# Performance work log

Measured on AMD Instinct MI355X. Metric: run time of the kernel, lower is better.

Reference implementation:

```python
import jax, jax.numpy as jnp
import numpy as np

B, S, H, E, K = 4, 2048, 1024, 8, 2
DFF = H * 8 // 3  # 2730, as in up: Linear(H, H*8//3)


def setup_inputs() -> dict:
    key = jax.random.key(0)
    ks = jax.random.split(key, 6)
    s = lambda fan: 1.0 / np.sqrt(fan)
    return {
        "x": jax.random.normal(ks[0], (B, S, H), jnp.float32),
        "Wr": jax.random.normal(ks[1], (H, E), jnp.float32) * s(H),
        "br": jnp.zeros((E,), jnp.float32),
        "Wg": jax.random.normal(ks[2], (E, H, H), jnp.float32) * s(H),
        "bg": jnp.zeros((E, H), jnp.float32),
        "Wu": jax.random.normal(ks[3], (E, H, DFF), jnp.float32) * s(H),
        "bu": jnp.zeros((E, DFF), jnp.float32),
        "Wd": jax.random.normal(ks[4], (E, DFF, H), jnp.float32) * s(DFF),
        "bd": jnp.zeros((E, H), jnp.float32),
    }


def reference(x, Wr, br, Wg, bg, Wu, bu, Wd, bd):
    b, s_, h = x.shape
    n = b * s_
    # Router: logits -> softmax -> top-k -> renormalize top-k weights
    expert_weight = x @ Wr + br                      # [B,S,E] (returned raw logits)
    logits_flat = expert_weight.reshape(n, -1)       # [N,E]
    probs = jax.nn.softmax(logits_flat, axis=-1)
    w, idx = jax.lax.top_k(probs, K)                 # [N,K]
    w = w / w.sum(axis=-1, keepdims=True)
    # Scatter top-k weights into dense [N,E] combine matrix (zeros elsewhere)
    rw = jnp.zeros_like(logits_flat).at[jnp.arange(n)[:, None], idx].add(w)
    # Expert MLP (BasicExpert): down(silu(up(gate(x)))); dropout is identity at eval
    xf = x.reshape(n, h)                             # [N,H]
    g = jnp.einsum("nh,ehf->enf", xf, Wg) + bg[:, None, :]       # [E,N,H]
    u = jax.nn.silu(jnp.einsum("enf,efd->end", g, Wu) + bu[:, None, :])  # [E,N,DFF]
    d = jnp.einsum("end,edh->enh", u, Wd) + bd[:, None, :]       # [E,N,H]
    # Combine: weighted sum over experts (weight is 0 for non-selected experts)
    y = jnp.einsum("enh,ne->nh", d, rw)
    return y.reshape(b, s_, h), expert_weight
```

## Files before the change

### kernel.cpp

```cpp
#include <hip/hip_runtime.h>
#include <hip/hip_bf16.h>

#define NB 4
#define SS 2048
#define HH 1024
#define EE 8
#define KK 2
#define DFF 2730
#define DFFP 2752
#define NT (NB*SS)
#define NA (NT*KK)
#define YSZ ((size_t)NT*HH)

using bf16x8 = __attribute__((ext_vector_type(8))) short;
using f32x4  = __attribute__((ext_vector_type(4))) float;

__device__ __forceinline__ ushort f2bf(float f) {
  unsigned u = __float_as_uint(f);
  unsigned r = (u + 0x7FFFu + ((u >> 16) & 1u)) >> 16;
  return (ushort)r;
}

__device__ __forceinline__ void gload16(const ushort* g, ushort* s) {
  __builtin_amdgcn_global_load_lds((const __attribute__((address_space(1))) void*)g,
                                   (__attribute__((address_space(3))) void*)s, 16, 0, 0);
}

__global__ __launch_bounds__(256) void cvt_w_kernel(const float4* __restrict__ in4,
                                                    ushort4* __restrict__ o4, int n4) {
  int i = blockIdx.x * 256 + threadIdx.x;
  if (i >= n4) return;
  float4 v = in4[i];
  ushort4 o;
  o.x = f2bf(v.x); o.y = f2bf(v.y); o.z = f2bf(v.z); o.w = f2bf(v.w);
  o4[i] = o;
}

__global__ __launch_bounds__(256) void transpose_cvt_kernel(
    const float* __restrict__ in, ushort* __restrict__ out,
    int K, int Nn, int Kpad, int Nnpad, long in_estride, long out_estride) {
  __shared__ float t[64][65];
  int e = blockIdx.z;
  const float* ine = in + (size_t)e * in_estride;
  ushort* oute = out + (size_t)e * out_estride;
  int nb = blockIdx.x * 64, kb = blockIdx.y * 64;
  int tid = threadIdx.x;
  int rr = tid >> 4, cc = (tid & 15) * 4;
  if (kb + 64 <= K && nb + 64 <= Nn) {
#pragma unroll
    for (int i = 0; i < 4; ++i) {
      int r = rr + i * 16;
      const float* src = ine + (size_t)(kb + r) * Nn + nb + cc;
      float2 a = *(const float2*)src;
      float2 b = *(const float2*)(src + 2);
      t[r][cc] = a.x; t[r][cc + 1] = a.y; t[r][cc + 2] = b.x; t[r][cc + 3] = b.y;
    }
  } else {
#pragma unroll
    for (int i = 0; i < 4; ++i) {
      int r = rr + i * 16;
      int kg = kb + r;
#pragma unroll
      for (int j = 0; j < 4; ++j) {
        int ng = nb + cc + j;
        t[r][cc + j] = (kg < K && ng < Nn) ? ine[(size_t)kg * Nn + ng] : 0.0f;
      }
    }
  }
  __syncthreads();
  int kq = tid & 15;
#pragma unroll
  for (int i = 0; i < 4; ++i) {
    int nl = rr + i * 16, ng = nb + nl;
    ushort4 v;
    v.x = f2bf(t[kq * 4 + 0][nl]);
    v.y = f2bf(t[kq * 4 + 1][nl]);
    v.z = f2bf(t[kq * 4 + 2][nl]);
    v.w = f2bf(t[kq * 4 + 3][nl]);
    *(ushort4*)&oute[(size_t)ng * Kpad + kb + kq * 4] = v;
  }
}

__global__ __launch_bounds__(256) void router_kernel(
    const float* __restrict__ x, const float* __restrict__ Wr, const float* __restrict__ br,
    float* __restrict__ logits_out, int* __restrict__ counts,
    int* __restrict__ tok_e, float* __restrict__ tok_w, ushort* __restrict__ xb) {
  int wv = threadIdx.x >> 6, l = threadIdx.x & 63;
  int n = blockIdx.x * 4 + wv;
  const float* xr = x + (size_t)n * HH;
  ushort* xbr = xb + (size_t)n * HH;
  float acc[8] = {0, 0, 0, 0, 0, 0, 0, 0};
#pragma unroll 4
  for (int i = 0; i < 16; ++i) {
    int k = l + i * 64;
    float xv = xr[k];
    xbr[k] = f2bf(xv);
    const float4* w4 = (const float4*)(Wr + (size_t)k * 8);
    float4 a = w4[0], b = w4[1];
    acc[0] += xv * a.x; acc[1] += xv * a.y; acc[2] += xv * a.z; acc[3] += xv * a.w;
    acc[4] += xv * b.x; acc[5] += xv * b.y; acc[6] += xv * b.z; acc[7] += xv * b.w;
  }
#pragma unroll
  for (int s = 1; s < 64; s <<= 1)
#pragma unroll
    for (int e2 = 0; e2 < 8; ++e2) acc[e2] += __shfl_xor(acc[e2], s);
#pragma unroll
  for (int e2 = 0; e2 < 8; ++e2) acc[e2] += br[e2];
  if (l < 8) logits_out[(size_t)n * 8 + l] = acc[l];
  if (l == 0) {
    int i0 = 0;
#pragma unroll
    for (int e2 = 1; e2 < 8; ++e2) if (acc[e2] > acc[i0]) i0 = e2;
    int i1 = (i0 == 0) ? 1 : 0;
#pragma unroll
    for (int e2 = 0; e2 < 8; ++e2) if (e2 != i0 && acc[e2] > acc[i1]) i1 = e2;
    float e10 = __expf(acc[i1] - acc[i0]);
    float w0 = 1.0f / (1.0f + e10);
    tok_e[2 * n] = i0; tok_e[2 * n + 1] = i1;
    tok_w[2 * n] = w0; tok_w[2 * n + 1] = e10 / (1.0f + e10);
    atomicAdd(&counts[i0], 1); atomicAdd(&counts[i1], 1);
  }
}

__global__ void prefix_kernel(const int* __restrict__ counts, int* __restrict__ bases,
                              int* __restrict__ cursor) {
  if (threadIdx.x == 0) {
    int s = 0;
    for (int e = 0; e < EE; ++e) { bases[e] = s; s += counts[e]; }
    bases[EE] = s;
  }
  if (threadIdx.x < EE) cursor[threadIdx.x] = 0;
}

__global__ __launch_bounds__(256) void scatter_kernel(
    const int* __restrict__ tok_e, const float* __restrict__ tok_w,
    const int* __restrict__ bases, int* __restrict__ cursor,
    int* __restrict__ assign_token, float* __restrict__ assign_w) {
  int n = blockIdx.x * 256 + threadIdx.x;
  if (n >= NT) return;
#pragma unroll
  for (int k2 = 0; k2 < 2; ++k2) {
    int e = tok_e[2 * n + k2];
    int pos = atomicAdd(&cursor[e], 1);
    int slot = bases[e] + pos;
    assign_token[slot] = n;
    assign_w[slot] = tok_w[2 * n + k2];
  }
}

__global__ __launch_bounds__(256) void bcomb_kernel(
    const ushort* __restrict__ wut, const float* __restrict__ bg,
    const float* __restrict__ bu, float* __restrict__ bc) {
  int gid = blockIdx.x * 4 + (threadIdx.x >> 6);
  int l = threadIdx.x & 63;
  int e = gid / DFFP, d = gid - e * DFFP;
  const ushort* row = wut + ((size_t)e * DFFP + d) * HH;
  const float* bge = bg + (size_t)e * HH;
  float s = 0.f;
#pragma unroll
  for (int i = 0; i < 4; ++i) {
    int k = (l + i * 64) * 4;
    ushort4 w4 = *(const ushort4*)&row[k];
    float4 b4 = *(const float4*)&bge[k];
    s += __uint_as_float((unsigned)w4.x << 16) * b4.x
       + __uint_as_float((unsigned)w4.y << 16) * b4.y
       + __uint_as_float((unsigned)w4.z << 16) * b4.z
       + __uint_as_float((unsigned)w4.w << 16) * b4.w;
  }
#pragma unroll
  for (int sh = 1; sh < 64; sh <<= 1) s += __shfl_xor(s, sh);
  if (l == 0) bc[(size_t)e * DFFP + d] = s + ((d < DFF) ? bu[(size_t)e * DFF + d] : 0.f);
}

template <int MODE, int MB, int NBT>
__global__ __launch_bounds__(256, 3) void moe_gemm_kernel(
    const ushort* __restrict__ Abase, const ushort* __restrict__ Wbase,
    const float* __restrict__ bias, ushort* __restrict__ outb, float* __restrict__ y,
    const int* __restrict__ bases, const int* __restrict__ assign_token,
    const float* __restrict__ assign_w,
    int K, int lda, long wstride_e, int bias_stride, int ldc,
    int ncols_valid, int ncols_write, int wrows) {
  constexpr int nwg = MB * NBT * EE;
  constexpr int q = nwg >> 3, r8 = nwg & 7;
  int orig = blockIdx.x;
  int xcd = orig & 7, pos = orig >> 3;
  int id = (xcd < r8 ? xcd * (q + 1) : r8 * (q + 1) + (xcd - r8) * q) + pos;
  int m = id % MB; int t2 = id / MB;
  int n = t2 % NBT;
  int e = t2 / NBT;

  int base, Ce;
  if (MODE == 3) { base = e * DFFP; Ce = DFFP; }
  else           { base = bases[e]; Ce = bases[e + 1] - base; }
  int m0 = m * 128;
  if (m0 >= Ce) return;
  int n0 = n * 128;
  int rows_valid = Ce - m0; if (rows_valid > 128) rows_valid = 128;

  __shared__ ushort lds[24576];
  int tid = threadIdx.x, w = tid >> 6, l = tid & 63;
  int wm = w >> 1, wn = w & 1;

  const ushort* aptr[2];
  const ushort* bptr[2];
  int lofs[2];
  const ushort* We = Wbase + (size_t)e * wstride_e;
  int csrc = ((l & 3) ^ ((l >> 3) & 3)) * 8;
#pragma unroll
  for (int i = 0; i < 2; ++i) {
    int r = i * 64 + w * 16 + (l >> 2);
    int ar = r < rows_valid ? r : rows_valid - 1;
    int slot = base + m0 + ar;
    long arow = (MODE == 4) ? (long)assign_token[slot] : (long)slot;
    aptr[i] = Abase + arow * (long)lda + csrc;
    int wr = n0 + r; if (wr >= wrows) wr = wrows - 1;
    bptr[i] = We + (size_t)wr * K + csrc;
    lofs[i] = (i * 256 + w * 64) * 8;
  }

  f32x4 acc[4][4];
#pragma unroll
  for (int a1 = 0; a1 < 4; ++a1)
#pragma unroll
    for (int b1 = 0; b1 < 4; ++b1) acc[a1][b1] = f32x4{0.f, 0.f, 0.f, 0.f};

  int nk = K >> 5;
#pragma unroll
  for (int i = 0; i < 2; ++i) {
    gload16(aptr[i], &lds[lofs[i]]);
    gload16(bptr[i], &lds[4096 + lofs[i]]);
  }
#pragma unroll
  for (int i = 0; i < 2; ++i) {
    gload16(aptr[i] + 32, &lds[8192 + lofs[i]]);
    gload16(bptr[i] + 32, &lds[8192 + 4096 + lofs[i]]);
  }

  int l15 = l & 15, lhi = l >> 4;
  int bc_ = 0, bs_ = 2;
  for (int t = 0; t < nk; ++t) {
    if (t + 1 < nk) {
      asm volatile("s_waitcnt vmcnt(4)" ::: "memory");
    } else {
      asm volatile("s_waitcnt vmcnt(0)" ::: "memory");
    }
    __builtin_amdgcn_s_barrier();
    if (t + 2 < nk) {
      int k0 = (t + 2) << 5;
      int sb = bs_ << 13;
#pragma unroll
      for (int i = 0; i < 2; ++i) {
        gload16(aptr[i] + k0, &lds[sb + lofs[i]]);
        gload16(bptr[i] + k0, &lds[sb + 4096 + lofs[i]]);
      }
    }
    const ushort* cA = &lds[bc_ << 13];
    const ushort* cB = &lds[(bc_ << 13) + 4096];
    bf16x8 af[4], bfr[4];
#pragma unroll
    for (int mt = 0; mt < 4; ++mt) {
      int row = wm * 64 + mt * 16 + l15;
      int cir = lhi ^ ((l15 >> 1) & 3);
      af[mt] = *(const bf16x8*)&cA[row * 32 + cir * 8];
    }
#pragma unroll
    for (int nt = 0; nt < 4; ++nt) {
      int row = wn * 64 + nt * 16 + l15;
      int cir = lhi ^ ((l15 >> 1) & 3);
      bfr[nt] = *(const bf16x8*)&cB[row * 32 + cir * 8];
    }
    __builtin_amdgcn_s_setprio(1);
#pragma unroll
    for (int mt = 0; mt < 4; ++mt)
#pragma unroll
      for (int nt = 0; nt < 4; ++nt)
        acc[mt][nt] = __builtin_amdgcn_mfma_f32_16x16x32_bf16(af[mt], bfr[nt], acc[mt][nt], 0, 0, 0);
    __builtin_amdgcn_s_setprio(0);
    int nb_ = bc_ + 1; if (nb_ == 3) nb_ = 0;
    int ns_ = bs_ + 1; if (ns_ == 3) ns_ = 0;
    bc_ = nb_; bs_ = ns_;
  }

  int lr = l >> 4, lc = l & 15;
#pragma unroll
  for (int mt = 0; mt < 4; ++mt) {
#pragma unroll
    for (int i2 = 0; i2 < 4; ++i2) {
      int r = wm * 64 + mt * 16 + lr * 4 + i2;
      if (r >= rows_valid) continue;
      int slot = base + m0 + r;
      int tok = 0; float wgt = 0.f;
      if (MODE == 2) { tok = assign_token[slot]; wgt = assign_w[slot]; }
#pragma unroll
      for (int nt = 0; nt < 4; ++nt) {
        int col = n0 + wn * 64 + nt * 16 + lc;
        if (col >= ncols_write) continue;
        float v = acc[mt][nt][i2];
        if (MODE == 3) {
          outb[(size_t)slot * ldc + col] = f2bf(v);
        } else if (MODE == 4) {
          float o = 0.0f;
          if (col < ncols_valid) {
            v += bias[(size_t)e * bias_stride + col];
            o = v / (1.0f + __expf(-v));
          }
          outb[(size_t)slot * ldc + col] = f2bf(o);
        } else {
          v += bias[(size_t)e * bias_stride + col];
          atomicAdd(&y[(size_t)tok * HH + col], wgt * v);
        }
      }
    }
  }
}

extern "C" void kernel_launch(void* const* d_in, const int* in_sizes, int n_in,
                              void* d_out, int out_size, void* d_ws, size_t ws_size,
                              hipStream_t stream) {
  const float* x  = (const float*)d_in[0];
  const float* Wr = (const float*)d_in[1];
  const float* br = (const float*)d_in[2];
  const float* Wg = (const float*)d_in[3];
  const float* bg = (const float*)d_in[4];
  const float* Wu = (const float*)d_in[5];
  const float* bu = (const float*)d_in[6];
  const float* Wd = (const float*)d_in[7];
  const float* bd = (const float*)d_in[8];
  float* y = (float*)d_out;
  float* logits = y + YSZ;

  char* ws = (char*)d_ws;
  size_t o = 0;
  auto alloc = [&](size_t b) { size_t r = o; o = (o + b + 255) & ~(size_t)255; return r; };
  size_t XB  = alloc((size_t)NT * HH * 2);
  size_t WGN = alloc((size_t)EE * HH * HH * 2);
  size_t WUT = alloc((size_t)EE * DFFP * HH * 2);
  size_t WDT = alloc((size_t)EE * HH * DFFP * 2);
  size_t WCB = alloc((size_t)EE * DFFP * HH * 2);
  size_t U   = alloc((size_t)NA * DFFP * 2);
  size_t BC  = alloc((size_t)EE * DFFP * 4);
  size_t META = alloc(262400);

  ushort* xb  = (ushort*)(ws + XB);
  ushort* wgn = (ushort*)(ws + WGN);
  ushort* wut = (ushort*)(ws + WUT);
  ushort* wdt = (ushort*)(ws + WDT);
  ushort* wcb = (ushort*)(ws + WCB);
  ushort* u   = (ushort*)(ws + U);
  float* bcomb = (float*)(ws + BC);
  int* meta = (int*)(ws + META);
  int* counts = meta;
  int* bases  = meta + 16;
  int* cursor = meta + 32;
  int* tok_e  = meta + 64;
  float* tok_w = (float*)(tok_e + NA);
  int* assign_token = (int*)(tok_w + NA);
  float* assign_w = (float*)(assign_token + NA);

  hipMemsetAsync(y, 0, YSZ * sizeof(float), stream);
  hipMemsetAsync(meta, 0, 256, stream);

  router_kernel<<<NT / 4, 256, 0, stream>>>(x, Wr, br, logits, counts, tok_e, tok_w, xb);
  cvt_w_kernel<<<(EE * HH * HH / 4 + 255) / 256, 256, 0, stream>>>(
      (const float4*)Wg, (ushort4*)wgn, EE * HH * HH / 4);
  transpose_cvt_kernel<<<dim3(DFFP / 64, 16, EE), 256, 0, stream>>>(Wu, wut, HH, DFF, HH, DFFP,
                                                                    (long)HH * DFF, (long)DFFP * HH);
  transpose_cvt_kernel<<<dim3(16, DFFP / 64, EE), 256, 0, stream>>>(Wd, wdt, DFF, HH, DFFP, HH,
                                                                    (long)DFF * HH, (long)HH * DFFP);
  prefix_kernel<<<1, 64, 0, stream>>>(counts, bases, cursor);
  scatter_kernel<<<NT / 256, 256, 0, stream>>>(tok_e, tok_w, bases, cursor, assign_token, assign_w);
  bcomb_kernel<<<EE * DFFP / 4, 256, 0, stream>>>(wut, bg, bu, bcomb);

  moe_gemm_kernel<3, 22, 8><<<22 * 8 * EE, 256, 0, stream>>>(
      wut, wgn, nullptr, wcb, nullptr, nullptr, nullptr, nullptr,
      HH, HH, (long)HH * HH, 0, HH, HH, HH, HH);
  moe_gemm_kernel<4, 17, 22><<<17 * 22 * EE, 256, 0, stream>>>(
      xb, wcb, bcomb, u, nullptr, bases, assign_token, nullptr,
      HH, HH, (long)DFFP * HH, DFFP, DFFP, DFF, DFFP, DFFP);
  moe_gemm_kernel<2, 17, 8><<<17 * 8 * EE, 256, 0, stream>>>(
      u, wdt, bd, nullptr, y, bases, assign_token, assign_w,
      DFFP, DFFP, (long)HH * DFFP, HH, HH, HH, HH, HH);
}
```

Before: 789.0 us.

## Widen MoE GEMM tiles to 128x256 with per-wave 128x64 output

Each workgroup of the grouped expert GEMM now computes a 128x256 output tile instead of 128x128. Each of the four waves owns a 128x64 slab with 8x4 MFMA accumulators, up from 4x4. LDS grows to three 24KB stages and the grid column counts are halved. The aim is more MFMA work per LDS fragment load and less redundant A-tile global traffic. The cost is higher register and LDS pressure, which lowers occupancy (launch bounds go from 3 to 2) and leaves fewer workgroups to fill the CUs.

New measurement: 845.8 us. +7.2%, slower.

```diff
diff --git a/kernel.cpp b/kernel.cpp
--- a/kernel.cpp
+++ b/kernel.cpp
@@ -173,7 +173,7 @@
 }
 
 template <int MODE, int MB, int NBT>
-__global__ __launch_bounds__(256, 3) void moe_gemm_kernel(
+__global__ __launch_bounds__(256, 2) void moe_gemm_kernel(
     const ushort* __restrict__ Abase, const ushort* __restrict__ Wbase,
     const float* __restrict__ bias, ushort* __restrict__ outb, float* __restrict__ y,
     const int* __restrict__ bases, const int* __restrict__ assign_token,
@@ -194,16 +194,15 @@
   else           { base = bases[e]; Ce = bases[e + 1] - base; }
   int m0 = m * 128;
   if (m0 >= Ce) return;
-  int n0 = n * 128;
+  int n0 = n * 256;
   int rows_valid = Ce - m0; if (rows_valid > 128) rows_valid = 128;
 
-  __shared__ ushort lds[24576];
+  __shared__ ushort lds[36864];
   int tid = threadIdx.x, w = tid >> 6, l = tid & 63;
-  int wm = w >> 1, wn = w & 1;
 
   const ushort* aptr[2];
-  const ushort* bptr[2];
-  int lofs[2];
+  const ushort* bptr[4];
+  int lofsA[2], lofsB[4];
   const ushort* We = Wbase + (size_t)e * wstride_e;
   int csrc = ((l & 3) ^ ((l >> 3) & 3)) * 8;
 #pragma unroll
@@ -213,65 +212,66 @@
     int slot = base + m0 + ar;
     long arow = (MODE == 4) ? (long)assign_token[slot] : (long)slot;
     aptr[i] = Abase + arow * (long)lda + csrc;
+    lofsA[i] = (i * 256 + w * 64) * 8;
+  }
+#pragma unroll
+  for (int i = 0; i < 4; ++i) {
+    int r = i * 64 + w * 16 + (l >> 2);
     int wr = n0 + r; if (wr >= wrows) wr = wrows - 1;
     bptr[i] = We + (size_t)wr * K + csrc;
-    lofs[i] = (i * 256 + w * 64) * 8;
-  }
-
-  f32x4 acc[4][4];
-#pragma unroll
-  for (int a1 = 0; a1 < 4; ++a1)
+    lofsB[i] = 4096 + (i * 256 + w * 64) * 8;
+  }
+
+  f32x4 acc[8][4];
+#pragma unroll
+  for (int a1 = 0; a1 < 8; ++a1)
 #pragma unroll
     for (int b1 = 0; b1 < 4; ++b1) acc[a1][b1] = f32x4{0.f, 0.f, 0.f, 0.f};
 
   int nk = K >> 5;
 #pragma unroll
-  for (int i = 0; i < 2; ++i) {
-    gload16(aptr[i], &lds[lofs[i]]);
-    gload16(bptr[i], &lds[4096 + lofs[i]]);
-  }
-#pragma unroll
-  for (int i = 0; i < 2; ++i) {
-    gload16(aptr[i] + 32, &lds[8192 + lofs[i]]);
-    gload16(bptr[i] + 32, &lds[8192 + 4096 + lofs[i]]);
-  }
+  for (int i = 0; i < 2; ++i) gload16(aptr[i], &lds[lofsA[i]]);
+#pragma unroll
+  for (int i = 0; i < 4; ++i) gload16(bptr[i], &lds[lofsB[i]]);
+#pragma unroll
+  for (int i = 0; i < 2; ++i) gload16(aptr[i] + 32, &lds[12288 + lofsA[i]]);
+#pragma unroll
+  for (int i = 0; i < 4; ++i) gload16(bptr[i] + 32, &lds[12288 + lofsB[i]]);
 
   int l15 = l & 15, lhi = l >> 4;
+  int cirx = (lhi ^ ((l15 >> 1) & 3)) * 8;
   int bc_ = 0, bs_ = 2;
   for (int t = 0; t < nk; ++t) {
     if (t + 1 < nk) {
-      asm volatile("s_waitcnt vmcnt(4)" ::: "memory");
+      asm volatile("s_waitcnt vmcnt(6)" ::: "memory");
     } else {
       asm volatile("s_waitcnt vmcnt(0)" ::: "memory");
     }
     __builtin_amdgcn_s_barrier();
     if (t + 2 < nk) {
       int k0 = (t + 2) << 5;
-      int sb = bs_ << 13;
-#pragma unroll
-      for (int i = 0; i < 2; ++i) {
-        gload16(aptr[i] + k0, &lds[sb + lofs[i]]);
-        gload16(bptr[i] + k0, &lds[sb + 4096 + lofs[i]]);
-      }
-    }
-    const ushort* cA = &lds[bc_ << 13];
-    const ushort* cB = &lds[(bc_ << 13) + 4096];
-    bf16x8 af[4], bfr[4];
-#pragma unroll
-    for (int mt = 0; mt < 4; ++mt) {
-      int row = wm * 64 + mt * 16 + l15;
-      int cir = lhi ^ ((l15 >> 1) & 3);
-      af[mt] = *(const bf16x8*)&cA[row * 32 + cir * 8];
+      int sb = bs_ * 12288;
+#pragma unroll
+      for (int i = 0; i < 2; ++i) gload16(aptr[i] + k0, &lds[sb + lofsA[i]]);
+#pragma unroll
+      for (int i = 0; i < 4; ++i) gload16(bptr[i] + k0, &lds[sb + lofsB[i]]);
+    }
+    const ushort* cA = &lds[bc_ * 12288];
+    const ushort* cB = &lds[bc_ * 12288 + 4096];
+    bf16x8 af[8], bfr[4];
+#pragma unroll
+    for (int mt = 0; mt < 8; ++mt) {
+      int row = mt * 16 + l15;
+      af[mt] = *(const bf16x8*)&cA[row * 32 + cirx];
     }
 #pragma unroll
     for (int nt = 0; nt < 4; ++nt) {
-      int row = wn * 64 + nt * 16 + l15;
-      int cir = lhi ^ ((l15 >> 1) & 3);
-      bfr[nt] = *(const bf16x8*)&cB[row * 32 + cir * 8];
+      int row = w * 64 + nt * 16 + l15;
+      bfr[nt] = *(const bf16x8*)&cB[row * 32 + cirx];
     }
     __builtin_amdgcn_s_setprio(1);
 #pragma unroll
-    for (int mt = 0; mt < 4; ++mt)
+    for (int mt = 0; mt < 8; ++mt)
 #pragma unroll
       for (int nt = 0; nt < 4; ++nt)
         acc[mt][nt] = __builtin_amdgcn_mfma_f32_16x16x32_bf16(af[mt], bfr[nt], acc[mt][nt], 0, 0, 0);
@@ -283,17 +283,17 @@
 
   int lr = l >> 4, lc = l & 15;
 #pragma unroll
-  for (int mt = 0; mt < 4; ++mt) {
+  for (int mt = 0; mt < 8; ++mt) {
 #pragma unroll
     for (int i2 = 0; i2 < 4; ++i2) {
-      int r = wm * 64 + mt * 16 + lr * 4 + i2;
+      int r = mt * 16 + lr * 4 + i2;
       if (r >= rows_valid) continue;
       int slot = base + m0 + r;
       int tok = 0; float wgt = 0.f;
       if (MODE == 2) { tok = assign_token[slot]; wgt = assign_w[slot]; }
 #pragma unroll
       for (int nt = 0; nt < 4; ++nt) {
-        int col = n0 + wn * 64 + nt * 16 + lc;
+        int col = n0 + w * 64 + nt * 16 + lc;
         if (col >= ncols_write) continue;
         float v = acc[mt][nt][i2];
         if (MODE == 3) {
@@ -371,13 +371,13 @@
   scatter_kernel<<<NT / 256, 256, 0, stream>>>(tok_e, tok_w, bases, cursor, assign_token, assign_w);
   bcomb_kernel<<<EE * DFFP / 4, 256, 0, stream>>>(wut, bg, bu, bcomb);
 
-  moe_gemm_kernel<3, 22, 8><<<22 * 8 * EE, 256, 0, stream>>>(
+  moe_gemm_kernel<3, 22, 4><<<22 * 4 * EE, 256, 0, stream>>>(
       wut, wgn, nullptr, wcb, nullptr, nullptr, nullptr, nullptr,
       HH, HH, (long)HH * HH, 0, HH, HH, HH, HH);
-  moe_gemm_kernel<4, 17, 22><<<17 * 22 * EE, 256, 0, stream>>>(
+  moe_gemm_kernel<4, 17, 11><<<17 * 11 * EE, 256, 0, stream>>>(
       xb, wcb, bcomb, u, nullptr, bases, assign_token, nullptr,
       HH, HH, (long)DFFP * HH, DFFP, DFFP, DFF, DFFP, DFFP);
-  moe_gemm_kernel<2, 17, 8><<<17 * 8 * EE, 256, 0, stream>>>(
+  moe_gemm_kernel<2, 17, 4><<<17 * 4 * EE, 256, 0, stream>>>(
       u, wdt, bd, nullptr, y, bases, assign_token, assign_w,
       DFFP, DFFP, (long)HH * DFFP, HH, HH, HH, HH, HH);
 }
```
